# Optimization experiments

Hardware: AMD Instinct MI355X
Metric: run time of the kernel (lower is better)

Reference implementation:

```python
import jax, jax.numpy as jnp
import numpy as np

E = 16          # number of experts
K = 2           # top-k routing
D = 1024        # model dim
F = 512         # expert ffn dim
T = 4096        # tokens
C = 2048


def setup_inputs() -> dict:
    key = jax.random.key(0)
    k1, k2, k3, k4, k5, k6 = jax.random.split(key, 6)
    return {
        "hidden_states": jax.random.normal(k1, (T, D), jnp.float32),
        "topk_indices": jax.random.randint(k2, (T, K), 0, E, jnp.int64),
        "topk_weights": jax.random.uniform(k3, (T, K), jnp.float32),
        "w_gate": jax.random.normal(k4, (E, D, F), jnp.float32) * 0.02,
        "w_up": jax.random.normal(k5, (E, D, F), jnp.float32) * 0.02,
        "w_down": jax.random.normal(k6, (E, F, D), jnp.float32) * 0.02,
    }


def reference(hidden_states, topk_indices, topk_weights, w_gate, w_up, w_down):
    Tn, d = hidden_states.shape
    k = topk_indices.shape[1]
    TK = Tn * k

    # ---- dispatch_tokens: group (token, expert) pairs by expert id ----
    flat_e = topk_indices.reshape(-1)                 # [TK] expert id per slot
    flat_w = topk_weights.reshape(-1)                 # [TK]
    flat_t = jnp.arange(TK) // k                      # [TK] source token id
    order = jnp.argsort(flat_e)                       # sort slots by expert
    se, st, sw = flat_e[order], flat_t[order], flat_w[order]
    counts = jnp.bincount(flat_e, length=E)           # tokens per expert
    starts = jnp.cumsum(counts) - counts              # exclusive prefix sum
    pos = jnp.arange(TK) - starts[se]                 # position within expert bucket
    valid = pos < C
    slot = jnp.where(valid, se * C + pos, E * C)      # overflow -> scratch row

    # gather tokens into padded per-expert buffers [E, C, D]
    buf = jnp.zeros((E * C + 1, d), hidden_states.dtype).at[slot].set(hidden_states[st])
    xe = buf[: E * C].reshape(E, C, d)

    # ---- per-expert gated-SiLU MLP via grouped GEMMs ----
    h = jax.nn.silu(jnp.einsum('ecd,edf->ecf', xe, w_gate)) * jnp.einsum('ecd,edf->ecf', xe, w_up)
    ye = jnp.einsum('ecf,efd->ecd', h, w_down).reshape(E * C, d)

    # ---- weighted scatter-add combine (index_add_) ----
    contrib = ye[jnp.minimum(slot, E * C - 1)] * (sw * valid.astype(sw.dtype))[:, None]
    out = jnp.zeros((Tn, d), topk_weights.dtype).at[st].add(contrib)
    return out.astype(hidden_states.dtype)
```

## Files before the change

kernel.cpp:

```cpp
#include <hip/hip_runtime.h>
#include <hip/hip_bf16.h>

constexpr int E_ = 16, K_ = 2, D_ = 1024, F_ = 512, T_ = 4096;
constexpr int TK_ = T_ * K_;
constexpr int CAP_ = 2048;
constexpr int BM_ = 128;
constexpr int ROWS_MAX = 10240;

constexpr size_t SZ_W   = (size_t)E_ * F_ * D_ * 2;
constexpr size_t OFF_WGT  = 0;
constexpr size_t OFF_WUT  = OFF_WGT + SZ_W;
constexpr size_t OFF_WDT  = OFF_WUT + SZ_W;
constexpr size_t OFF_XG   = OFF_WDT + SZ_W;
constexpr size_t SZ_XG  = (size_t)ROWS_MAX * D_ * 2;
constexpr size_t OFF_H    = OFF_XG + SZ_XG;
constexpr size_t SZ_H   = (size_t)ROWS_MAX * F_ * 2;
constexpr size_t OFF_META = OFF_H + SZ_H;

typedef __attribute__((ext_vector_type(8))) short short8;
typedef __attribute__((ext_vector_type(4))) float float4v;

__device__ __forceinline__ unsigned short f2bf(float f) {
  union { float f; unsigned int u; } v; v.f = f;
  unsigned int r = (v.u + 0x7fffu + ((v.u >> 16) & 1u)) >> 16;
  return (unsigned short)r;
}

__device__ __forceinline__ void load_lds16(const unsigned short* g, unsigned short* l) {
  __builtin_amdgcn_global_load_lds(
      (const __attribute__((address_space(1))) unsigned int*)g,
      (__attribute__((address_space(3))) unsigned int*)l,
      16, 0, 0);
}

__launch_bounds__(1024)
__global__ void dispatch_k(const int* __restrict__ idx, const float* __restrict__ tw,
                           int* __restrict__ cnt_c, int* __restrict__ off_al,
                           int* __restrict__ row_token, float* __restrict__ row_weight) {
  __shared__ int hist[E_], offs[E_], ctr[E_];
  int tid = threadIdx.x;
  if (tid < E_) hist[tid] = 0;
  __syncthreads();
  for (int i = tid; i < TK_; i += 1024) atomicAdd(&hist[idx[i]], 1);
  __syncthreads();
  if (tid == 0) {
    int run = 0;
    for (int e = 0; e < E_; ++e) {
      int c = hist[e] > CAP_ ? CAP_ : hist[e];
      cnt_c[e] = c; off_al[e] = run; offs[e] = run; ctr[e] = 0;
      run += (c + BM_ - 1) & ~(BM_ - 1);
    }
  }
  __syncthreads();
  for (int r = tid; r < ROWS_MAX; r += 1024) row_token[r] = -1;
  __syncthreads();
  for (int i = tid; i < TK_; i += 1024) {
    int e = idx[i];
    int r = atomicAdd(&ctr[e], 1);
    if (r < CAP_) {
      int row = offs[e] + r;
      row_token[row] = i >> 1;
      row_weight[row] = tw[i];
    }
  }
}

__global__ void gather_k(const float* __restrict__ hidden, const int* __restrict__ row_token,
                         unsigned short* __restrict__ Xg) {
  int r = blockIdx.x;
  int tok = row_token[r];
  int c = threadIdx.x * 4;
  ushort4 o;
  if (tok >= 0) {
    float4 v = *(const float4*)(hidden + (size_t)tok * D_ + c);
    o.x = f2bf(v.x); o.y = f2bf(v.y); o.z = f2bf(v.z); o.w = f2bf(v.w);
  } else {
    o.x = 0; o.y = 0; o.z = 0; o.w = 0;
  }
  *(ushort4*)(Xg + (size_t)r * D_ + c) = o;
}

__global__ void transpose_all_k(const float* __restrict__ wg, const float* __restrict__ wu,
                                const float* __restrict__ wd,
                                unsigned short* __restrict__ WgT, unsigned short* __restrict__ WuT,
                                unsigned short* __restrict__ WdT) {
  __shared__ float tile[32][33];
  int z = blockIdx.y;
  int kind = z >> 4, e = z & 15;
  int R = (kind == 2) ? F_ : D_;
  int C = (kind == 2) ? D_ : F_;
  const float* s = ((kind == 0) ? wg : (kind == 1) ? wu : wd) + (size_t)e * R * C;
  unsigned short* d = ((kind == 0) ? WgT : (kind == 1) ? WuT : WdT) + (size_t)e * R * C;
  int tilesX = C >> 5;
  int t = blockIdx.x;
  int r0 = (t / tilesX) * 32, c0 = (t % tilesX) * 32;
  int tr = threadIdx.x >> 3;
  int tc = (threadIdx.x & 7) * 4;
  float4 v = *(const float4*)(s + (size_t)(r0 + tr) * C + (c0 + tc));
  tile[tr][tc + 0] = v.x; tile[tr][tc + 1] = v.y;
  tile[tr][tc + 2] = v.z; tile[tr][tc + 3] = v.w;
  __syncthreads();
  ushort4 o;
  o.x = f2bf(tile[tc + 0][tr]);
  o.y = f2bf(tile[tc + 1][tr]);
  o.z = f2bf(tile[tc + 2][tr]);
  o.w = f2bf(tile[tc + 3][tr]);
  *(ushort4*)(d + (size_t)(c0 + tr) * R + (r0 + tc)) = o;
}


__launch_bounds__(256)
__global__ void gemm1_k(const unsigned short* __restrict__ Xg,
                        const unsigned short* __restrict__ WgT,
                        const unsigned short* __restrict__ WuT,
                        unsigned short* __restrict__ Hbuf,
                        const int* __restrict__ cnt_c, const int* __restrict__ off_al) {
  int e = blockIdx.z, mt = blockIdx.y, nt = blockIdx.x;
  int cnt = cnt_c[e];
  if (mt * 128 >= cnt) return;
  int rbase = off_al[e] + mt * 128;

  __shared__ unsigned short lA[128 * 64];
  __shared__ unsigned short lBg[64 * 64];
  __shared__ unsigned short lBu[64 * 64];

  int tid = threadIdx.x, wid = tid >> 6, lane = tid & 63;
  int wm = wid >> 1, wn = wid & 1;
  int quad = lane >> 4, l15 = lane & 15;
  int sw = l15 & 7;

  const unsigned short* gA = Xg + (size_t)rbase * D_;
  const unsigned short* gB0 = WgT + ((size_t)e * F_ + nt * 64) * D_;
  const unsigned short* gB1 = WuT + ((size_t)e * F_ + nt * 64) * D_;

  float4v accg[4][2], accu[4][2];
#pragma unroll
  for (int i = 0; i < 4; ++i)
#pragma unroll
    for (int j = 0; j < 2; ++j) {
      accg[i][j] = (float4v){0.f, 0.f, 0.f, 0.f};
      accu[i][j] = (float4v){0.f, 0.f, 0.f, 0.f};
    }

  for (int k0 = 0; k0 < D_; k0 += 64) {
    __syncthreads();
#pragma unroll
    for (int it = 0; it < 4; ++it) {
      int fw = it * 256 + wid * 64;
      int f = fw + lane;
      int row = f >> 3, c8 = (f & 7) ^ (row & 7);
      load_lds16(gA + (size_t)row * D_ + k0 + c8 * 8, &lA[(size_t)fw * 8]);
    }
#pragma unroll
    for (int it = 0; it < 2; ++it) {
      int fw = it * 256 + wid * 64;
      int f = fw + lane;
      int row = f >> 3, c8 = (f & 7) ^ (row & 7);
      size_t go = (size_t)row * D_ + k0 + c8 * 8;
      load_lds16(gB0 + go, &lBg[(size_t)fw * 8]);
      load_lds16(gB1 + go, &lBu[(size_t)fw * 8]);
    }
    __syncthreads();
#pragma unroll
    for (int kc = 0; kc < 2; ++kc) {
      short8 af[4], bg[2], bu[2];
#pragma unroll
      for (int i = 0; i < 4; ++i) {
        int r = wm * 64 + i * 16 + l15;
        af[i] = *(const short8*)&lA[r * 64 + ((kc * 4 + quad) ^ sw) * 8];
      }
#pragma unroll
      for (int j = 0; j < 2; ++j) {
        int n = wn * 32 + j * 16 + l15;
        bg[j] = *(const short8*)&lBg[n * 64 + ((kc * 4 + quad) ^ sw) * 8];
        bu[j] = *(const short8*)&lBu[n * 64 + ((kc * 4 + quad) ^ sw) * 8];
      }
#pragma unroll
      for (int i = 0; i < 4; ++i)
#pragma unroll
        for (int j = 0; j < 2; ++j) {
          accg[i][j] = __builtin_amdgcn_mfma_f32_16x16x32_bf16(af[i], bg[j], accg[i][j], 0, 0, 0);
          accu[i][j] = __builtin_amdgcn_mfma_f32_16x16x32_bf16(af[i], bu[j], accu[i][j], 0, 0, 0);
        }
    }
  }

  int rem = cnt - mt * 128;
#pragma unroll
  for (int i = 0; i < 4; ++i)
#pragma unroll
    for (int j = 0; j < 2; ++j)
#pragma unroll
      for (int r = 0; r < 4; ++r) {
        int row = wm * 64 + i * 16 + quad * 4 + r;
        if (row < rem) {
          float g = accg[i][j][r], u = accu[i][j][r];
          float h = (g / (1.f + __expf(-g))) * u;
          int n = nt * 64 + wn * 32 + j * 16 + l15;
          Hbuf[(size_t)(rbase + row) * F_ + n] = f2bf(h);
        }
      }
}

__launch_bounds__(256)
__global__ void gemm2_k(const unsigned short* __restrict__ Hbuf,
                        const unsigned short* __restrict__ WdT,
                        float* __restrict__ out,
                        const int* __restrict__ cnt_c, const int* __restrict__ off_al,
                        const int* __restrict__ row_token, const float* __restrict__ row_weight) {
  int e = blockIdx.z, mt = blockIdx.y, nt = blockIdx.x;
  int cnt = cnt_c[e];
  if (mt * 128 >= cnt) return;
  int rbase = off_al[e] + mt * 128;

  __shared__ unsigned short lA[128 * 64];
  __shared__ unsigned short lB[128 * 64];

  int tid = threadIdx.x, wid = tid >> 6, lane = tid & 63;
  int wm = wid >> 1, wn = wid & 1;
  int quad = lane >> 4, l15 = lane & 15;
  int sw = l15 & 7;

  const unsigned short* gA = Hbuf + (size_t)rbase * F_;
  const unsigned short* gB = WdT + ((size_t)e * D_ + nt * 128) * F_;

  float4v acc[4][4];
#pragma unroll
  for (int i = 0; i < 4; ++i)
#pragma unroll
    for (int j = 0; j < 4; ++j) acc[i][j] = (float4v){0.f, 0.f, 0.f, 0.f};

  for (int k0 = 0; k0 < F_; k0 += 64) {
    __syncthreads();
#pragma unroll
    for (int it = 0; it < 4; ++it) {
      int fw = it * 256 + wid * 64;
      int f = fw + lane;
      int row = f >> 3, c8 = (f & 7) ^ (row & 7);
      size_t go = (size_t)row * F_ + k0 + c8 * 8;
      load_lds16(gA + go, &lA[(size_t)fw * 8]);
      load_lds16(gB + go, &lB[(size_t)fw * 8]);
    }
    __syncthreads();
#pragma unroll
    for (int kc = 0; kc < 2; ++kc) {
      short8 af[4], bf[4];
#pragma unroll
      for (int i = 0; i < 4; ++i) {
        int r = wm * 64 + i * 16 + l15;
        af[i] = *(const short8*)&lA[r * 64 + ((kc * 4 + quad) ^ sw) * 8];
      }
#pragma unroll
      for (int j = 0; j < 4; ++j) {
        int n = wn * 64 + j * 16 + l15;
        bf[j] = *(const short8*)&lB[n * 64 + ((kc * 4 + quad) ^ sw) * 8];
      }
#pragma unroll
      for (int i = 0; i < 4; ++i)
#pragma unroll
        for (int j = 0; j < 4; ++j)
          acc[i][j] = __builtin_amdgcn_mfma_f32_16x16x32_bf16(af[i], bf[j], acc[i][j], 0, 0, 0);
    }
  }

  int rem = cnt - mt * 128;
#pragma unroll
  for (int i = 0; i < 4; ++i)
#pragma unroll
    for (int r = 0; r < 4; ++r) {
      int row = wm * 64 + i * 16 + quad * 4 + r;
      if (row < rem) {
        int gr = rbase + row;
        int tok = row_token[gr];
        if (tok >= 0) {
          float w = row_weight[gr];
          float* op = out + (size_t)tok * D_;
#pragma unroll
          for (int j = 0; j < 4; ++j) {
            int n = nt * 128 + wn * 64 + j * 16 + l15;
            atomicAdd(op + n, w * acc[i][j][r]);
          }
        }
      }
    }
}

extern "C" void kernel_launch(void* const* d_in, const int* in_sizes, int n_in,
                              void* d_out, int out_size, void* d_ws, size_t ws_size,
                              hipStream_t stream) {
  const float* hidden  = (const float*)d_in[0];
  const int*   topkidx = (const int*)d_in[1];
  const float* topkw   = (const float*)d_in[2];
  const float* w_gate  = (const float*)d_in[3];
  const float* w_up    = (const float*)d_in[4];
  const float* w_down  = (const float*)d_in[5];
  float* out = (float*)d_out;

  char* ws = (char*)d_ws;
  unsigned short* WgT = (unsigned short*)(ws + OFF_WGT);
  unsigned short* WuT = (unsigned short*)(ws + OFF_WUT);
  unsigned short* WdT = (unsigned short*)(ws + OFF_WDT);
  unsigned short* Xg  = (unsigned short*)(ws + OFF_XG);
  unsigned short* Hb  = (unsigned short*)(ws + OFF_H);
  int* meta           = (int*)(ws + OFF_META);
  int* cnt_c    = meta;
  int* off_al   = meta + 16;
  int* row_token = meta + 32;
  float* row_weight = (float*)(meta + 32 + ROWS_MAX);

  hipMemsetAsync(out, 0, (size_t)out_size * sizeof(float), stream);

  dispatch_k<<<1, 1024, 0, stream>>>(topkidx, topkw, cnt_c, off_al, row_token, row_weight);
  transpose_all_k<<<dim3(512, 48), 256, 0, stream>>>(w_gate, w_up, w_down, WgT, WuT, WdT);
  gather_k<<<ROWS_MAX, 256, 0, stream>>>(hidden, row_token, Xg);

  gemm1_k<<<dim3(F_ / 64, CAP_ / 128, E_), 256, 0, stream>>>(Xg, WgT, WuT, Hb, cnt_c, off_al);
  gemm2_k<<<dim3(D_ / 128, CAP_ / 128, E_), 256, 0, stream>>>(Hb, WdT, out, cnt_c, off_al,
                                                              row_token, row_weight);
}
```

Before: 270.8 us.

## Parallelize dispatch, double-buffer grouped GEMMs with smaller M tiles and swizzled grid

Result: slower. 290.4 us (+7.2%).

```diff
diff --git a/kernel.cpp b/kernel.cpp
--- a/kernel.cpp
+++ b/kernel.cpp
@@ -33,35 +33,34 @@
       16, 0, 0);
 }
 
-__launch_bounds__(1024)
-__global__ void dispatch_k(const int* __restrict__ idx, const float* __restrict__ tw,
-                           int* __restrict__ cnt_c, int* __restrict__ off_al,
-                           int* __restrict__ row_token, float* __restrict__ row_weight) {
-  __shared__ int hist[E_], offs[E_], ctr[E_];
-  int tid = threadIdx.x;
-  if (tid < E_) hist[tid] = 0;
-  __syncthreads();
-  for (int i = tid; i < TK_; i += 1024) atomicAdd(&hist[idx[i]], 1);
-  __syncthreads();
-  if (tid == 0) {
+__global__ void hist_k(const int* __restrict__ idx, int* __restrict__ hist) {
+  int i = blockIdx.x * blockDim.x + threadIdx.x;
+  if (i < TK_) atomicAdd(&hist[idx[i]], 1);
+}
+
+__global__ void scan_k(const int* __restrict__ hist, int* __restrict__ cnt_c,
+                       int* __restrict__ off_al, int* __restrict__ ctr) {
+  if (threadIdx.x == 0) {
     int run = 0;
     for (int e = 0; e < E_; ++e) {
       int c = hist[e] > CAP_ ? CAP_ : hist[e];
-      cnt_c[e] = c; off_al[e] = run; offs[e] = run; ctr[e] = 0;
+      cnt_c[e] = c; off_al[e] = run; ctr[e] = 0;
       run += (c + BM_ - 1) & ~(BM_ - 1);
     }
   }
-  __syncthreads();
-  for (int r = tid; r < ROWS_MAX; r += 1024) row_token[r] = -1;
-  __syncthreads();
-  for (int i = tid; i < TK_; i += 1024) {
-    int e = idx[i];
-    int r = atomicAdd(&ctr[e], 1);
-    if (r < CAP_) {
-      int row = offs[e] + r;
-      row_token[row] = i >> 1;
-      row_weight[row] = tw[i];
-    }
+}
+
+__global__ void assign_k(const int* __restrict__ idx, const float* __restrict__ tw,
+                         const int* __restrict__ off_al, int* __restrict__ ctr,
+                         int* __restrict__ row_token, float* __restrict__ row_weight) {
+  int i = blockIdx.x * blockDim.x + threadIdx.x;
+  if (i >= TK_) return;
+  int e = idx[i];
+  int r = atomicAdd(&ctr[e], 1);
+  if (r < CAP_) {
+    int row = off_al[e] + r;
+    row_token[row] = i >> 1;
+    row_weight[row] = tw[i];
   }
 }
 
@@ -115,14 +114,16 @@
                         const unsigned short* __restrict__ WuT,
                         unsigned short* __restrict__ Hbuf,
                         const int* __restrict__ cnt_c, const int* __restrict__ off_al) {
-  int e = blockIdx.z, mt = blockIdx.y, nt = blockIdx.x;
+  int bid = blockIdx.x;
+  int swz = (bid & 7) * 512 + (bid >> 3);
+  int e = swz >> 8, mt = (swz >> 3) & 31, nt = swz & 7;
   int cnt = cnt_c[e];
-  if (mt * 128 >= cnt) return;
-  int rbase = off_al[e] + mt * 128;
-
-  __shared__ unsigned short lA[128 * 64];
-  __shared__ unsigned short lBg[64 * 64];
-  __shared__ unsigned short lBu[64 * 64];
+  if (mt * 64 >= cnt) return;
+  int rbase = off_al[e] + mt * 64;
+
+  __shared__ unsigned short lA[2][64 * 64];
+  __shared__ unsigned short lBg[2][64 * 64];
+  __shared__ unsigned short lBu[2][64 * 64];
 
   int tid = threadIdx.x, wid = tid >> 6, lane = tid & 63;
   int wm = wid >> 1, wn = wid & 1;
@@ -133,66 +134,67 @@
   const unsigned short* gB0 = WgT + ((size_t)e * F_ + nt * 64) * D_;
   const unsigned short* gB1 = WuT + ((size_t)e * F_ + nt * 64) * D_;
 
-  float4v accg[4][2], accu[4][2];
-#pragma unroll
-  for (int i = 0; i < 4; ++i)
+  float4v accg[2][2], accu[2][2];
+#pragma unroll
+  for (int i = 0; i < 2; ++i)
 #pragma unroll
     for (int j = 0; j < 2; ++j) {
       accg[i][j] = (float4v){0.f, 0.f, 0.f, 0.f};
       accu[i][j] = (float4v){0.f, 0.f, 0.f, 0.f};
     }
 
-  for (int k0 = 0; k0 < D_; k0 += 64) {
-    __syncthreads();
-#pragma unroll
-    for (int it = 0; it < 4; ++it) {
-      int fw = it * 256 + wid * 64;
-      int f = fw + lane;
-      int row = f >> 3, c8 = (f & 7) ^ (row & 7);
-      load_lds16(gA + (size_t)row * D_ + k0 + c8 * 8, &lA[(size_t)fw * 8]);
-    }
+  auto stage = [&](int buf, int k0) {
 #pragma unroll
     for (int it = 0; it < 2; ++it) {
       int fw = it * 256 + wid * 64;
       int f = fw + lane;
       int row = f >> 3, c8 = (f & 7) ^ (row & 7);
       size_t go = (size_t)row * D_ + k0 + c8 * 8;
-      load_lds16(gB0 + go, &lBg[(size_t)fw * 8]);
-      load_lds16(gB1 + go, &lBu[(size_t)fw * 8]);
-    }
-    __syncthreads();
+      load_lds16(gA + go, &lA[buf][fw * 8]);
+      load_lds16(gB0 + go, &lBg[buf][fw * 8]);
+      load_lds16(gB1 + go, &lBu[buf][fw * 8]);
+    }
+  };
+
+  stage(0, 0);
+  __syncthreads();
+
+  for (int kt = 0; kt < 16; ++kt) {
+    int cur = kt & 1;
+    if (kt + 1 < 16) stage(cur ^ 1, (kt + 1) * 64);
 #pragma unroll
     for (int kc = 0; kc < 2; ++kc) {
-      short8 af[4], bg[2], bu[2];
-#pragma unroll
-      for (int i = 0; i < 4; ++i) {
-        int r = wm * 64 + i * 16 + l15;
-        af[i] = *(const short8*)&lA[r * 64 + ((kc * 4 + quad) ^ sw) * 8];
+      short8 af[2], bg[2], bu[2];
+#pragma unroll
+      for (int i = 0; i < 2; ++i) {
+        int r = wm * 32 + i * 16 + l15;
+        af[i] = *(const short8*)&lA[cur][r * 64 + ((kc * 4 + quad) ^ sw) * 8];
       }
 #pragma unroll
       for (int j = 0; j < 2; ++j) {
         int n = wn * 32 + j * 16 + l15;
-        bg[j] = *(const short8*)&lBg[n * 64 + ((kc * 4 + quad) ^ sw) * 8];
-        bu[j] = *(const short8*)&lBu[n * 64 + ((kc * 4 + quad) ^ sw) * 8];
-      }
-#pragma unroll
-      for (int i = 0; i < 4; ++i)
+        bg[j] = *(const short8*)&lBg[cur][n * 64 + ((kc * 4 + quad) ^ sw) * 8];
+        bu[j] = *(const short8*)&lBu[cur][n * 64 + ((kc * 4 + quad) ^ sw) * 8];
+      }
+#pragma unroll
+      for (int i = 0; i < 2; ++i)
 #pragma unroll
         for (int j = 0; j < 2; ++j) {
           accg[i][j] = __builtin_amdgcn_mfma_f32_16x16x32_bf16(af[i], bg[j], accg[i][j], 0, 0, 0);
           accu[i][j] = __builtin_amdgcn_mfma_f32_16x16x32_bf16(af[i], bu[j], accu[i][j], 0, 0, 0);
         }
     }
-  }
-
-  int rem = cnt - mt * 128;
-#pragma unroll
-  for (int i = 0; i < 4; ++i)
+    __syncthreads();
+  }
+
+  int rem = cnt - mt * 64;
+#pragma unroll
+  for (int i = 0; i < 2; ++i)
 #pragma unroll
     for (int j = 0; j < 2; ++j)
 #pragma unroll
       for (int r = 0; r < 4; ++r) {
-        int row = wm * 64 + i * 16 + quad * 4 + r;
+        int row = wm * 32 + i * 16 + quad * 4 + r;
         if (row < rem) {
           float g = accg[i][j][r], u = accu[i][j][r];
           float h = (g / (1.f + __expf(-g))) * u;
@@ -208,13 +210,15 @@
                         float* __restrict__ out,
                         const int* __restrict__ cnt_c, const int* __restrict__ off_al,
                         const int* __restrict__ row_token, const float* __restrict__ row_weight) {
-  int e = blockIdx.z, mt = blockIdx.y, nt = blockIdx.x;
+  int bid = blockIdx.x;
+  int swz = (bid & 7) * 512 + (bid >> 3);
+  int e = swz >> 8, mt = (swz >> 3) & 31, nt = swz & 7;
   int cnt = cnt_c[e];
-  if (mt * 128 >= cnt) return;
-  int rbase = off_al[e] + mt * 128;
-
-  __shared__ unsigned short lA[128 * 64];
-  __shared__ unsigned short lB[128 * 64];
+  if (mt * 64 >= cnt) return;
+  int rbase = off_al[e] + mt * 64;
+
+  __shared__ unsigned short lA[2][64 * 64];
+  __shared__ unsigned short lB[2][128 * 64];
 
   int tid = threadIdx.x, wid = tid >> 6, lane = tid & 63;
   int wm = wid >> 1, wn = wid & 1;
@@ -224,51 +228,63 @@
   const unsigned short* gA = Hbuf + (size_t)rbase * F_;
   const unsigned short* gB = WdT + ((size_t)e * D_ + nt * 128) * F_;
 
-  float4v acc[4][4];
-#pragma unroll
-  for (int i = 0; i < 4; ++i)
+  float4v acc[2][4];
+#pragma unroll
+  for (int i = 0; i < 2; ++i)
 #pragma unroll
     for (int j = 0; j < 4; ++j) acc[i][j] = (float4v){0.f, 0.f, 0.f, 0.f};
 
-  for (int k0 = 0; k0 < F_; k0 += 64) {
-    __syncthreads();
+  auto stage = [&](int buf, int k0) {
+#pragma unroll
+    for (int it = 0; it < 2; ++it) {
+      int fw = it * 256 + wid * 64;
+      int f = fw + lane;
+      int row = f >> 3, c8 = (f & 7) ^ (row & 7);
+      load_lds16(gA + (size_t)row * F_ + k0 + c8 * 8, &lA[buf][fw * 8]);
+    }
 #pragma unroll
     for (int it = 0; it < 4; ++it) {
       int fw = it * 256 + wid * 64;
       int f = fw + lane;
       int row = f >> 3, c8 = (f & 7) ^ (row & 7);
-      size_t go = (size_t)row * F_ + k0 + c8 * 8;
-      load_lds16(gA + go, &lA[(size_t)fw * 8]);
-      load_lds16(gB + go, &lB[(size_t)fw * 8]);
-    }
-    __syncthreads();
+      load_lds16(gB + (size_t)row * F_ + k0 + c8 * 8, &lB[buf][fw * 8]);
+    }
+  };
+
+  stage(0, 0);
+  __syncthreads();
+
+  for (int kt = 0; kt < 8; ++kt) {
+    int cur = kt & 1;
+    if (kt + 1 < 8) stage(cur ^ 1, (kt + 1) * 64);
 #pragma unroll
     for (int kc = 0; kc < 2; ++kc) {
-      short8 af[4], bf[4];
-#pragma unroll
-      for (int i = 0; i < 4; ++i) {
-        int r = wm * 64 + i * 16 + l15;
-        af[i] = *(const short8*)&lA[r * 64 + ((kc * 4 + quad) ^ sw) * 8];
+      short8 af[2], bf[4];
+#pragma unroll
+      for (int i = 0; i < 2; ++i) {
+        int r = wm * 32 + i * 16 + l15;
+        af[i] = *(const short8*)&lA[cur][r * 64 + ((kc * 4 + quad) ^ sw) * 8];
       }
 #pragma unroll
       for (int j = 0; j < 4; ++j) {
         int n = wn * 64 + j * 16 + l15;
-        bf[j] = *(const short8*)&lB[n * 64 + ((kc * 4 + quad) ^ sw) * 8];
-      }
-#pragma unroll
-      for (int i = 0; i < 4; ++i)
+        bf[j] = *(const short8*)&lB[cur][n * 64 + ((kc * 4 + quad) ^ sw) * 8];
+      }
+#pragma unroll
+      for (int i = 0; i < 2; ++i)
 #pragma unroll
         for (int j = 0; j < 4; ++j)
           acc[i][j] = __builtin_amdgcn_mfma_f32_16x16x32_bf16(af[i], bf[j], acc[i][j], 0, 0, 0);
     }
-  }
-
-  int rem = cnt - mt * 128;
-#pragma unroll
-  for (int i = 0; i < 4; ++i)
+    __syncthreads();
+  }
+
+  int rem = cnt - mt * 64;
+#pragma unroll
+  for (int i = 0; i < 2; ++i)
 #pragma unroll
     for (int r = 0; r < 4; ++r) {
-      int row = wm * 64 + i * 16 + quad * 4 + r;
+      int row = wm * 32 + i * 16 + quad * 4 + r;
       if (row < rem) {
         int gr = rbase + row;
         int tok = row_token[gr];
@@ -303,18 +319,24 @@
   unsigned short* Xg  = (unsigned short*)(ws + OFF_XG);
   unsigned short* Hb  = (unsigned short*)(ws + OFF_H);
   int* meta           = (int*)(ws + OFF_META);
-  int* cnt_c    = meta;
-  int* off_al   = meta + 16;
+  int* cnt_c     = meta;
+  int* off_al    = meta + 16;
   int* row_token = meta + 32;
   float* row_weight = (float*)(meta + 32 + ROWS_MAX);
+  int* hist      = meta + 32 + 2 * ROWS_MAX;
+  int* ctr       = hist + 16;
 
   hipMemsetAsync(out, 0, (size_t)out_size * sizeof(float), stream);
-
-  dispatch_k<<<1, 1024, 0, stream>>>(topkidx, topkw, cnt_c, off_al, row_token, row_weight);
+  hipMemsetAsync(hist, 0, 16 * sizeof(int), stream);
+  hipMemsetAsync(row_token, 0xFF, (size_t)ROWS_MAX * sizeof(int), stream);
+
+  hist_k<<<TK_ / 256, 256, 0, stream>>>(topkidx, hist);
+  scan_k<<<1, 64, 0, stream>>>(hist, cnt_c, off_al, ctr);
+  assign_k<<<TK_ / 256, 256, 0, stream>>>(topkidx, topkw, off_al, ctr, row_token, row_weight);
+
   transpose_all_k<<<dim3(512, 48), 256, 0, stream>>>(w_gate, w_up, w_down, WgT, WuT, WdT);
   gather_k<<<ROWS_MAX, 256, 0, stream>>>(hidden, row_token, Xg);
 
-  gemm1_k<<<dim3(F_ / 64, CAP_ / 128, E_), 256, 0, stream>>>(Xg, WgT, WuT, Hb, cnt_c, off_al);
-  gemm2_k<<<dim3(D_ / 128, CAP_ / 128, E_), 256, 0, stream>>>(Hb, WdT, out, cnt_c, off_al,
-                                                              row_token, row_weight);
-}
+  gemm1_k<<<4096, 256, 0, stream>>>(Xg, WgT, WuT, Hb, cnt_c, off_al);
+  gemm2_k<<<4096, 256, 0, stream>>>(Hb, WdT, out, cnt_c, off_al, row_token, row_weight);
+}
```
